# Kernel optimization log

Hardware: AMD Instinct MI355X
Metric: run time of the kernel (lower is better)

Reference implementation:

```python
import jax, jax.numpy as jnp
import numpy as np

HEADS = 16
D_MODEL = 1024
HEAD_DIM = D_MODEL // HEADS
NEG = -1e15


def setup_inputs() -> dict:
    key = jax.random.key(0)
    ks = jax.random.split(key, 13)
    B, L = 2, 2048
    scale = 1.0 / np.sqrt(D_MODEL)
    inp = {
        'q': jax.random.normal(ks[0], (B, L, D_MODEL), jnp.float32),
        'k': jax.random.normal(ks[1], (B, L, D_MODEL), jnp.float32),
        'v': jax.random.normal(ks[2], (B, L, D_MODEL), jnp.float32),
        'mask': jax.random.randint(ks[3], (B, 1, 1, L), 0, 2, jnp.int32),
        'Wq': jax.random.normal(ks[4], (D_MODEL, D_MODEL), jnp.float32) * scale,
        'bq': jax.random.normal(ks[5], (D_MODEL,), jnp.float32) * scale,
        'Wk': jax.random.normal(ks[6], (D_MODEL, D_MODEL), jnp.float32) * scale,
        'bk': jax.random.normal(ks[7], (D_MODEL,), jnp.float32) * scale,
        'Wv': jax.random.normal(ks[8], (D_MODEL, D_MODEL), jnp.float32) * scale,
        'bv': jax.random.normal(ks[9], (D_MODEL,), jnp.float32) * scale,
        'Wo': jax.random.normal(ks[10], (D_MODEL, D_MODEL), jnp.float32) * scale,
        'bo': jax.random.normal(ks[11], (D_MODEL,), jnp.float32) * scale,
    }
    return inp


def _split_heads(x):
    B, L, _ = x.shape
    return x.reshape(B, L, HEADS, HEAD_DIM).transpose(0, 2, 1, 3)  # [B,H,L,Dh]


def reference(q, k, v, mask, Wq, bq, Wk, bk, Wv, bv, Wo, bo):
    B, L, _ = q.shape
    # torch Linear: y = x @ W.T + b
    qh = _split_heads(q @ Wq.T + bq)
    kh = _split_heads(k @ Wk.T + bk)
    vh = _split_heads(v @ Wv.T + bv)
    scores = jnp.einsum('bhqd,bhkd->bhqk', qh, kh) / jnp.sqrt(jnp.float32(HEAD_DIM))
    scores = scores + mask.astype(scores.dtype) * NEG
    weights = jax.nn.softmax(scores, axis=-1)
    attn = jnp.einsum('bhqk,bhkd->bhqd', weights, vh)  # [B,H,L,Dh]
    attn = attn.transpose(0, 2, 1, 3).reshape(B, L, D_MODEL)
    return attn @ Wo.T + bo
```

## Files before the change

kernel.cpp:

```cpp
#include <hip/hip_runtime.h>
#include <stdint.h>

typedef __bf16 bf16;
typedef __attribute__((ext_vector_type(8))) __bf16 bf16x8;
typedef __attribute__((ext_vector_type(4))) __bf16 bf16x4;
typedef __attribute__((ext_vector_type(4))) float f32x4;

#define SEQ   2048
#define DM    1024
#define NH    16
#define HD    64
#define MROWS 4096

__device__ __forceinline__ void glds16(const bf16* g, bf16* l) {
  __builtin_amdgcn_global_load_lds(
      (__attribute__((address_space(1))) unsigned int*)(g),
      (__attribute__((address_space(3))) unsigned int*)(l),
      16, 0, 0);
}

static __device__ __forceinline__ bf16x8 cvt_f32x8(const float* __restrict__ p) {
  const f32x4 a = *(const f32x4*)p;
  const f32x4 b = *(const f32x4*)(p + 4);
  bf16x8 r;
  r[0] = (bf16)a[0]; r[1] = (bf16)a[1]; r[2] = (bf16)a[2]; r[3] = (bf16)a[3];
  r[4] = (bf16)b[0]; r[5] = (bf16)b[1]; r[6] = (bf16)b[2]; r[7] = (bf16)b[3];
  return r;
}

__global__ void conv_all(
    const float* __restrict__ q, const float* __restrict__ k, const float* __restrict__ v,
    const float* __restrict__ wq, const float* __restrict__ wk,
    const float* __restrict__ wv, const float* __restrict__ wo,
    bf16* __restrict__ dq, bf16* __restrict__ dk, bf16* __restrict__ dv,
    bf16* __restrict__ dwq, bf16* __restrict__ dwk, bf16* __restrict__ dwv,
    bf16* __restrict__ dwo)
{
  const size_t c = (size_t)blockIdx.x * 256 + threadIdx.x;
  const float* s; bf16* d; size_t off;
  if (c < 524288)        { s = q;  d = dq;  off = c; }
  else if (c < 1048576)  { s = k;  d = dk;  off = c - 524288; }
  else if (c < 1572864)  { s = v;  d = dv;  off = c - 1048576; }
  else if (c < 1703936)  { s = wq; d = dwq; off = c - 1572864; }
  else if (c < 1835008)  { s = wk; d = dwk; off = c - 1703936; }
  else if (c < 1966080)  { s = wv; d = dwv; off = c - 1835008; }
  else                   { s = wo; d = dwo; off = c - 1966080; }
  *(bf16x8*)(d + off * 8) = cvt_f32x8(s + off * 8);
}

__global__ __launch_bounds__(256, 4) void proj_qkv(
    const bf16* __restrict__ qb, const bf16* __restrict__ kb, const bf16* __restrict__ vb,
    const bf16* __restrict__ Wqb, const bf16* __restrict__ Wkb, const bf16* __restrict__ Wvb,
    const float* __restrict__ bq, const float* __restrict__ bk, const float* __restrict__ bv,
    bf16* __restrict__ Qh, bf16* __restrict__ Kh, bf16* __restrict__ Vt)
{
  __shared__ __align__(16) bf16 sA[128 * 64];
  __shared__ __align__(16) bf16 sB[128 * 64];

  const int z = blockIdx.z;
  const int o = (int)blockIdx.x + 8 * (int)blockIdx.y;
  const int rt = (o & 7) * 4 + ((o >> 3) & 3);
  const int ot = o >> 5;

  const bf16 *A, *B;
  const float* Bv;
  int m0, n0;
  if (z == 0)      { A = qb;  B = Wqb; Bv = bq; m0 = rt * 128; n0 = ot * 128; }
  else if (z == 1) { A = kb;  B = Wkb; Bv = bk; m0 = rt * 128; n0 = ot * 128; }
  else             { A = Wvb; B = vb;  Bv = bv; m0 = ot * 128; n0 = rt * 128; }

  const int tid  = threadIdx.x;
  const int lane = tid & 63;
  const int wv   = tid >> 6;
  const int quad = lane >> 4;
  const int colx = lane & 15;
  const int rm = (wv >> 1) * 64;
  const int rn = (wv & 1) * 64;

  f32x4 acc[4][4];
#pragma unroll
  for (int mi = 0; mi < 4; ++mi)
#pragma unroll
    for (int ni = 0; ni < 4; ++ni) {
      f32x4 zz = {0.f, 0.f, 0.f, 0.f};
      acc[mi][ni] = zz;
    }

  for (int kt = 0; kt < 16; ++kt) {
    const int k0 = kt * 64;
    __syncthreads();
#pragma unroll
    for (int i = 0; i < 4; ++i) {
      const int f = i * 256 + tid;
      const int row = f >> 3;
      const int cc = (f & 7) ^ (row & 7);
      glds16(A + (size_t)(m0 + row) * DM + k0 + cc * 8, sA + f * 8);
      glds16(B + (size_t)(n0 + row) * DM + k0 + cc * 8, sB + f * 8);
    }
    __syncthreads();

    bf16x8 af[4][2], bfr[4][2];
#pragma unroll
    for (int t4 = 0; t4 < 4; ++t4) {
#pragma unroll
      for (int ks = 0; ks < 2; ++ks) {
        const int ra = rm + t4 * 16 + colx;
        af[t4][ks] = *(const bf16x8*)(sA + ra * 64 + (((ks * 4 + quad) ^ (ra & 7)) * 8));
        const int rb = rn + t4 * 16 + colx;
        bfr[t4][ks] = *(const bf16x8*)(sB + rb * 64 + (((ks * 4 + quad) ^ (rb & 7)) * 8));
      }
    }
#pragma unroll
    for (int mi = 0; mi < 4; ++mi)
#pragma unroll
      for (int ni = 0; ni < 4; ++ni) {
        acc[mi][ni] = __builtin_amdgcn_mfma_f32_16x16x32_bf16(af[mi][0], bfr[ni][0], acc[mi][ni], 0, 0, 0);
        acc[mi][ni] = __builtin_amdgcn_mfma_f32_16x16x32_bf16(af[mi][1], bfr[ni][1], acc[mi][ni], 0, 0, 0);
      }
  }

  if (z == 2) {
#pragma unroll
    for (int mi = 0; mi < 4; ++mi) {
#pragma unroll
      for (int r = 0; r < 4; ++r) {
        const int m = m0 + rm + mi * 16 + quad * 4 + r;
        const float bias = Bv[m];
        const int hh = m >> 6, d = m & 63;
#pragma unroll
        for (int ni = 0; ni < 4; ++ni) {
          const int n = n0 + rn + ni * 16 + colx;
          const int b = n >> 11, l = n & 2047;
          Vt[(((size_t)(b * NH + hh) * HD + d) * SEQ) + l] =
              (bf16)(acc[mi][ni][r] + bias);
        }
      }
    }
  } else {
    bf16* Out = (z == 0) ? Qh : Kh;
    const float scale = (z == 0) ? 0.18033688f : 1.0f;
#pragma unroll
    for (int ni = 0; ni < 4; ++ni) {
      const int n = n0 + rn + ni * 16 + colx;
      const float bias = Bv[n];
#pragma unroll
      for (int mi = 0; mi < 4; ++mi) {
#pragma unroll
        for (int r = 0; r < 4; ++r) {
          const int m = m0 + rm + mi * 16 + quad * 4 + r;
          const float v = (acc[mi][ni][r] + bias) * scale;
          const int b = m >> 11, l = m & 2047, hh = n >> 6, d = n & 63;
          Out[((size_t)(b * NH + hh) * SEQ + l) * HD + d] = (bf16)v;
        }
      }
    }
  }
}

__global__ __launch_bounds__(256, 4) void proj_out(
    const bf16* __restrict__ At, const bf16* __restrict__ Wob,
    const float* __restrict__ bo, float* __restrict__ Out)
{
  __shared__ __align__(16) bf16 sA[128 * 64];
  __shared__ __align__(16) bf16 sB[128 * 64];

  const int o = (int)blockIdx.x + 8 * (int)blockIdx.y;
  const int m0 = ((o & 7) * 4 + ((o >> 3) & 3)) * 128;
  const int n0 = (o >> 5) * 128;

  const int tid  = threadIdx.x;
  const int lane = tid & 63;
  const int wv   = tid >> 6;
  const int quad = lane >> 4;
  const int colx = lane & 15;
  const int rm = (wv >> 1) * 64;
  const int rn = (wv & 1) * 64;

  f32x4 acc[4][4];
#pragma unroll
  for (int mi = 0; mi < 4; ++mi)
#pragma unroll
    for (int ni = 0; ni < 4; ++ni) {
      f32x4 zz = {0.f, 0.f, 0.f, 0.f};
      acc[mi][ni] = zz;
    }

  for (int kt = 0; kt < 16; ++kt) {
    const int k0 = kt * 64;
    __syncthreads();
#pragma unroll
    for (int i = 0; i < 4; ++i) {
      const int f = i * 256 + tid;
      const int row = f >> 3;
      const int cc = (f & 7) ^ (row & 7);
      glds16(At  + (size_t)(m0 + row) * DM + k0 + cc * 8, sA + f * 8);
      glds16(Wob + (size_t)(n0 + row) * DM + k0 + cc * 8, sB + f * 8);
    }
    __syncthreads();

    bf16x8 af[4][2], bfr[4][2];
#pragma unroll
    for (int t4 = 0; t4 < 4; ++t4) {
#pragma unroll
      for (int ks = 0; ks < 2; ++ks) {
        const int ra = rm + t4 * 16 + colx;
        af[t4][ks] = *(const bf16x8*)(sA + ra * 64 + (((ks * 4 + quad) ^ (ra & 7)) * 8));
        const int rb = rn + t4 * 16 + colx;
        bfr[t4][ks] = *(const bf16x8*)(sB + rb * 64 + (((ks * 4 + quad) ^ (rb & 7)) * 8));
      }
    }
#pragma unroll
    for (int mi = 0; mi < 4; ++mi)
#pragma unroll
      for (int ni = 0; ni < 4; ++ni) {
        acc[mi][ni] = __builtin_amdgcn_mfma_f32_16x16x32_bf16(af[mi][0], bfr[ni][0], acc[mi][ni], 0, 0, 0);
        acc[mi][ni] = __builtin_amdgcn_mfma_f32_16x16x32_bf16(af[mi][1], bfr[ni][1], acc[mi][ni], 0, 0, 0);
      }
  }

#pragma unroll
  for (int ni = 0; ni < 4; ++ni) {
    const int n = n0 + rn + ni * 16 + colx;
    const float bias = bo[n];
#pragma unroll
    for (int mi = 0; mi < 4; ++mi) {
#pragma unroll
      for (int r = 0; r < 4; ++r) {
        const int m = m0 + rm + mi * 16 + quad * 4 + r;
        Out[(size_t)m * DM + n] = acc[mi][ni][r] + bias;
      }
    }
  }
}

__global__ __launch_bounds__(256, 3) void attn_kernel(
    const bf16* __restrict__ Qh, const bf16* __restrict__ Kh, const bf16* __restrict__ Vt,
    const int* __restrict__ mask, bf16* __restrict__ At)
{
  __shared__ __align__(16) float sRed[64 * 68];
  __shared__ float sDen[64];

  const int tid  = threadIdx.x;
  const int lane = tid & 63;
  const int wv   = tid >> 6;
  const int quad = lane >> 4;
  const int colx = lane & 15;
  const int bh = blockIdx.x;
  const int b  = bh >> 4;
  const int h  = bh & 15;
  const int q0 = blockIdx.y * 64;
  const size_t base  = (size_t)bh * SEQ * HD;
  const size_t baseV = (size_t)bh * HD * SEQ;

  bf16x8 qf[4][2];
#pragma unroll
  for (int qg = 0; qg < 4; ++qg) {
    const int qrow = q0 + qg * 16 + colx;
    qf[qg][0] = *(const bf16x8*)(Qh + base + (size_t)qrow * HD + quad * 8);
    qf[qg][1] = *(const bf16x8*)(Qh + base + (size_t)qrow * HD + 32 + quad * 8);
  }

  f32x4 o[4][4];
  float osum[4];
#pragma unroll
  for (int qg = 0; qg < 4; ++qg) {
    osum[qg] = 0.f;
#pragma unroll
    for (int dt = 0; dt < 4; ++dt) {
      f32x4 zz = {0.f, 0.f, 0.f, 0.f};
      o[qg][dt] = zz;
    }
  }

  union VV { bf16x8 v8; bf16x4 v4[2]; };

  for (int t = 0; t < 16; ++t) {
    const int kb = t * 128 + wv * 32;

    bf16x8 kf[2][2];
#pragma unroll
    for (int g = 0; g < 2; ++g) {
#pragma unroll
      for (int ks = 0; ks < 2; ++ks)
        kf[g][ks] = *(const bf16x8*)(Kh + base + (size_t)(kb + g * 16 + colx) * HD + ks * 32 + quad * 8);
    }
    const int4 m0 = *(const int4*)(mask + b * SEQ + kb + quad * 4);
    const int4 m1 = *(const int4*)(mask + b * SEQ + kb + 16 + quad * 4);
    VV vvp[4];
#pragma unroll
    for (int dt = 0; dt < 4; ++dt) {
      const bf16* vrow = Vt + baseV + (size_t)(dt * 16 + colx) * SEQ + kb + quad * 4;
      vvp[dt].v4[0] = *(const bf16x4*)(vrow);
      vvp[dt].v4[1] = *(const bf16x4*)(vrow + 16);
    }

    float mr0[4], mr1[4];
    mr0[0] = (m0.x ? -1e30f : 0.0f) - 23.0830917f;
    mr0[1] = (m0.y ? -1e30f : 0.0f) - 23.0830917f;
    mr0[2] = (m0.z ? -1e30f : 0.0f) - 23.0830917f;
    mr0[3] = (m0.w ? -1e30f : 0.0f) - 23.0830917f;
    mr1[0] = (m1.x ? -1e30f : 0.0f) - 23.0830917f;
    mr1[1] = (m1.y ? -1e30f : 0.0f) - 23.0830917f;
    mr1[2] = (m1.z ? -1e30f : 0.0f) - 23.0830917f;
    mr1[3] = (m1.w ? -1e30f : 0.0f) - 23.0830917f;

    VV pa[4];
    __builtin_amdgcn_s_setprio(1);
#pragma unroll
    for (int qg = 0; qg < 4; ++qg) {
      f32x4 s = {0.f, 0.f, 0.f, 0.f};
      s = __builtin_amdgcn_mfma_f32_16x16x32_bf16(kf[0][0], qf[qg][0], s, 0, 0, 0);
      s = __builtin_amdgcn_mfma_f32_16x16x32_bf16(kf[0][1], qf[qg][1], s, 0, 0, 0);
#pragma unroll
      for (int r = 0; r < 4; ++r) {
        const float e = __builtin_amdgcn_exp2f(s[r] + mr0[r]);
        pa[qg].v8[r] = (bf16)e;
        osum[qg] += e;
      }
    }
#pragma unroll
    for (int qg = 0; qg < 4; ++qg) {
      f32x4 s = {0.f, 0.f, 0.f, 0.f};
      s = __builtin_amdgcn_mfma_f32_16x16x32_bf16(kf[1][0], qf[qg][0], s, 0, 0, 0);
      s = __builtin_amdgcn_mfma_f32_16x16x32_bf16(kf[1][1], qf[qg][1], s, 0, 0, 0);
#pragma unroll
      for (int r = 0; r < 4; ++r) {
        const float e = __builtin_amdgcn_exp2f(s[r] + mr1[r]);
        pa[qg].v8[4 + r] = (bf16)e;
        osum[qg] += e;
      }
    }

#pragma unroll
    for (int dt = 0; dt < 4; ++dt) {
#pragma unroll
      for (int qg = 0; qg < 4; ++qg)
        o[qg][dt] = __builtin_amdgcn_mfma_f32_16x16x32_bf16(pa[qg].v8, vvp[dt].v8, o[qg][dt], 0, 0, 0);
    }
    __builtin_amdgcn_s_setprio(0);
  }

#pragma unroll
  for (int qg = 0; qg < 4; ++qg) {
    osum[qg] += __shfl_xor(osum[qg], 16);
    osum[qg] += __shfl_xor(osum[qg], 32);
  }
  const float myden = (quad == 0) ? osum[0] : (quad == 1) ? osum[1]
                    : (quad == 2) ? osum[2] : osum[3];

#pragma unroll
  for (int p = 0; p < 4; ++p) {
    if (wv == p) {
#pragma unroll
      for (int qg = 0; qg < 4; ++qg)
#pragma unroll
        for (int dt = 0; dt < 4; ++dt) {
          float* a = &sRed[(dt * 16 + colx) * 68 + qg * 16 + quad * 4];
          if (p == 0) {
            *(f32x4*)a = o[qg][dt];
          } else {
            f32x4 c = *(const f32x4*)a;
            c += o[qg][dt];
            *(f32x4*)a = c;
          }
        }
      if (p == 0) sDen[quad * 16 + colx] = myden;
      else        sDen[quad * 16 + colx] += myden;
    }
    __syncthreads();
  }

  const float inv = 1.0f / sDen[wv * 16 + colx];
  bf16x8 out0, out1;
#pragma unroll
  for (int j = 0; j < 8; ++j) {
    out0[j] = (bf16)(sRed[(quad * 16 + j) * 68 + wv * 16 + colx] * inv);
    out1[j] = (bf16)(sRed[(quad * 16 + 8 + j) * 68 + wv * 16 + colx] * inv);
  }
  const size_t orow = ((size_t)(b * SEQ + q0 + wv * 16 + colx)) * DM + h * HD + quad * 16;
  *(bf16x8*)(At + orow) = out0;
  *(bf16x8*)(At + orow + 8) = out1;
}

extern "C" void kernel_launch(void* const* d_in, const int* in_sizes, int n_in,
                              void* d_out, int out_size, void* d_ws, size_t ws_size,
                              hipStream_t stream) {
  (void)in_sizes; (void)n_in; (void)out_size; (void)ws_size;
  const float* q    = (const float*)d_in[0];
  const float* k    = (const float*)d_in[1];
  const float* v    = (const float*)d_in[2];
  const int*   mask = (const int*)d_in[3];
  const float* Wq   = (const float*)d_in[4];
  const float* bq   = (const float*)d_in[5];
  const float* Wk   = (const float*)d_in[6];
  const float* bk   = (const float*)d_in[7];
  const float* Wv   = (const float*)d_in[8];
  const float* bv   = (const float*)d_in[9];
  const float* Wo   = (const float*)d_in[10];
  const float* bo   = (const float*)d_in[11];
  float* out = (float*)d_out;

  const size_t T = (size_t)MROWS * DM;
  const size_t WT = (size_t)DM * DM;
  bf16* ws  = (bf16*)d_ws;
  bf16* qb  = ws;
  bf16* kb  = qb + T;
  bf16* vb  = kb + T;
  bf16* Wqb = vb + T;
  bf16* Wkb = Wqb + WT;
  bf16* Wvb = Wkb + WT;
  bf16* Wob = Wvb + WT;
  bf16* Qh  = Wob + WT;
  bf16* Kh  = Qh + T;
  bf16* Vt  = Kh + T;
  bf16* At  = qb;

  dim3 blk(256);
  conv_all<<<8192, blk, 0, stream>>>(q, k, v, Wq, Wk, Wv, Wo,
                                     qb, kb, vb, Wqb, Wkb, Wvb, Wob);
  proj_qkv<<<dim3(8, 32, 3), blk, 0, stream>>>(qb, kb, vb, Wqb, Wkb, Wvb,
                                               bq, bk, bv, Qh, Kh, Vt);
  attn_kernel<<<dim3(32, 32), blk, 0, stream>>>(Qh, Kh, Vt, mask, At);
  proj_out<<<dim3(8, 32), blk, 0, stream>>>(At, Wob, bo, out);
}
```

Before: 259.6 us.

## Stage K/V tiles in LDS via async global_load_lds with XOR swizzle

```diff
diff --git a/kernel.cpp b/kernel.cpp
--- a/kernel.cpp
+++ b/kernel.cpp
@@ -131,7 +131,9 @@
         for (int ni = 0; ni < 4; ++ni) {
           const int n = n0 + rn + ni * 16 + colx;
           const int b = n >> 11, l = n & 2047;
-          Vt[(((size_t)(b * NH + hh) * HD + d) * SEQ) + l] =
+          const int lb = l >> 7, li = l & 127;
+          const int perm = (li & 96) | ((li & 12) << 1) | ((li & 16) >> 2) | (li & 3);
+          Vt[(((size_t)(b * NH + hh) * HD + d) * SEQ) + lb * 128 + perm] =
               (bf16)(acc[mi][ni][r] + bias);
         }
       }
@@ -237,8 +239,9 @@
     const bf16* __restrict__ Qh, const bf16* __restrict__ Kh, const bf16* __restrict__ Vt,
     const int* __restrict__ mask, bf16* __restrict__ At)
 {
-  __shared__ __align__(16) float sRed[64 * 68];
-  __shared__ float sDen[64];
+  __shared__ __align__(16) char smem[32768];
+  bf16* sK = (bf16*)smem;
+  bf16* sV = (bf16*)(smem + 16384);
 
   const int tid  = threadIdx.x;
   const int lane = tid & 63;
@@ -275,70 +278,71 @@
   union VV { bf16x8 v8; bf16x4 v4[2]; };
 
   for (int t = 0; t < 16; ++t) {
-    const int kb = t * 128 + wv * 32;
-
-    bf16x8 kf[2][2];
-#pragma unroll
-    for (int g = 0; g < 2; ++g) {
-#pragma unroll
-      for (int ks = 0; ks < 2; ++ks)
-        kf[g][ks] = *(const bf16x8*)(Kh + base + (size_t)(kb + g * 16 + colx) * HD + ks * 32 + quad * 8);
-    }
-    const int4 m0 = *(const int4*)(mask + b * SEQ + kb + quad * 4);
-    const int4 m1 = *(const int4*)(mask + b * SEQ + kb + 16 + quad * 4);
-    VV vvp[4];
-#pragma unroll
-    for (int dt = 0; dt < 4; ++dt) {
-      const bf16* vrow = Vt + baseV + (size_t)(dt * 16 + colx) * SEQ + kb + quad * 4;
-      vvp[dt].v4[0] = *(const bf16x4*)(vrow);
-      vvp[dt].v4[1] = *(const bf16x4*)(vrow + 16);
-    }
-
+    const int key0 = t * 128;
+    __syncthreads();
+#pragma unroll
+    for (int i = 0; i < 4; ++i) {
+      const int f = i * 256 + tid;
+      const int kr = f >> 3;
+      const int ck = (f & 7) ^ (kr & 7);
+      glds16(Kh + base + (size_t)(key0 + kr) * HD + ck * 8, sK + f * 8);
+      const int dr = f >> 4;
+      const int cv = (f & 15) ^ (dr & 15);
+      glds16(Vt + baseV + (size_t)dr * SEQ + key0 + cv * 8, sV + f * 8);
+    }
+    const int kb = key0 + wv * 32;
+    const int4 mA = *(const int4*)(mask + b * SEQ + kb + quad * 4);
+    const int4 mB = *(const int4*)(mask + b * SEQ + kb + 16 + quad * 4);
     float mr0[4], mr1[4];
-    mr0[0] = (m0.x ? -1e30f : 0.0f) - 23.0830917f;
-    mr0[1] = (m0.y ? -1e30f : 0.0f) - 23.0830917f;
-    mr0[2] = (m0.z ? -1e30f : 0.0f) - 23.0830917f;
-    mr0[3] = (m0.w ? -1e30f : 0.0f) - 23.0830917f;
-    mr1[0] = (m1.x ? -1e30f : 0.0f) - 23.0830917f;
-    mr1[1] = (m1.y ? -1e30f : 0.0f) - 23.0830917f;
-    mr1[2] = (m1.z ? -1e30f : 0.0f) - 23.0830917f;
-    mr1[3] = (m1.w ? -1e30f : 0.0f) - 23.0830917f;
+    mr0[0] = (mA.x ? -1e30f : 0.0f) - 23.0830917f;
+    mr0[1] = (mA.y ? -1e30f : 0.0f) - 23.0830917f;
+    mr0[2] = (mA.z ? -1e30f : 0.0f) - 23.0830917f;
+    mr0[3] = (mA.w ? -1e30f : 0.0f) - 23.0830917f;
+    mr1[0] = (mB.x ? -1e30f : 0.0f) - 23.0830917f;
+    mr1[1] = (mB.y ? -1e30f : 0.0f) - 23.0830917f;
+    mr1[2] = (mB.z ? -1e30f : 0.0f) - 23.0830917f;
+    mr1[3] = (mB.w ? -1e30f : 0.0f) - 23.0830917f;
+    __syncthreads();
 
     VV pa[4];
     __builtin_amdgcn_s_setprio(1);
 #pragma unroll
-    for (int qg = 0; qg < 4; ++qg) {
-      f32x4 s = {0.f, 0.f, 0.f, 0.f};
-      s = __builtin_amdgcn_mfma_f32_16x16x32_bf16(kf[0][0], qf[qg][0], s, 0, 0, 0);
-      s = __builtin_amdgcn_mfma_f32_16x16x32_bf16(kf[0][1], qf[qg][1], s, 0, 0, 0);
-#pragma unroll
-      for (int r = 0; r < 4; ++r) {
-        const float e = __builtin_amdgcn_exp2f(s[r] + mr0[r]);
-        pa[qg].v8[r] = (bf16)e;
-        osum[qg] += e;
-      }
-    }
-#pragma unroll
-    for (int qg = 0; qg < 4; ++qg) {
-      f32x4 s = {0.f, 0.f, 0.f, 0.f};
-      s = __builtin_amdgcn_mfma_f32_16x16x32_bf16(kf[1][0], qf[qg][0], s, 0, 0, 0);
-      s = __builtin_amdgcn_mfma_f32_16x16x32_bf16(kf[1][1], qf[qg][1], s, 0, 0, 0);
-#pragma unroll
-      for (int r = 0; r < 4; ++r) {
-        const float e = __builtin_amdgcn_exp2f(s[r] + mr1[r]);
-        pa[qg].v8[4 + r] = (bf16)e;
-        osum[qg] += e;
-      }
-    }
-
+    for (int g = 0; g < 2; ++g) {
+      const int krow = wv * 32 + g * 16 + colx;
+      const bf16x8 kfa = *(const bf16x8*)(sK + krow * 64 + ((quad ^ (krow & 7)) * 8));
+      const bf16x8 kfb = *(const bf16x8*)(sK + krow * 64 + (((4 + quad) ^ (krow & 7)) * 8));
+#pragma unroll
+      for (int qg = 0; qg < 4; ++qg) {
+        f32x4 s = {0.f, 0.f, 0.f, 0.f};
+        s = __builtin_amdgcn_mfma_f32_16x16x32_bf16(kfa, qf[qg][0], s, 0, 0, 0);
+        s = __builtin_amdgcn_mfma_f32_16x16x32_bf16(kfb, qf[qg][1], s, 0, 0, 0);
+#pragma unroll
+        for (int r = 0; r < 4; ++r) {
+          const float e = __builtin_amdgcn_exp2f(s[r] + (g ? mr1[r] : mr0[r]));
+          pa[qg].v8[g * 4 + r] = (bf16)e;
+          osum[qg] += e;
+        }
+      }
+    }
+
+    bf16x8 vf[4];
 #pragma unroll
     for (int dt = 0; dt < 4; ++dt) {
+      const int row = dt * 16 + colx;
+      vf[dt] = *(const bf16x8*)(sV + row * 128 + (((wv * 4 + quad) ^ colx) * 8));
+    }
+
+#pragma unroll
+    for (int dt = 0; dt < 4; ++dt)
 #pragma unroll
       for (int qg = 0; qg < 4; ++qg)
-        o[qg][dt] = __builtin_amdgcn_mfma_f32_16x16x32_bf16(pa[qg].v8, vvp[dt].v8, o[qg][dt], 0, 0, 0);
-    }
+        o[qg][dt] = __builtin_amdgcn_mfma_f32_16x16x32_bf16(pa[qg].v8, vf[dt], o[qg][dt], 0, 0, 0);
     __builtin_amdgcn_s_setprio(0);
   }
+
+  __syncthreads();
+  float* sRed = (float*)smem;
+  float* sDen = (float*)(smem + 64 * 68 * 4);
 
 #pragma unroll
   for (int qg = 0; qg < 4; ++qg) {
```

Result: faster. 245.0 us (-5.6%).
